# Performance work log

Measured on AMD Instinct MI355X. Metric: run time of the kernel, lower is better.

## Reference

```python
import jax, jax.numpy as jnp
from jax import lax
import numpy as np

NEG = -10000.0

def sequence_mask(length, max_len):
    # [B, max_len] bool
    return jnp.arange(max_len)[None, :] < length[:, None]

def mdn_loss(logp, text_lengths, mel_lengths):
    # logp: [B, T_seq, T_mel]; CTC-style forward recursion over T_mel
    B, T_seq, T_mel = logp.shape
    init = jnp.full((B, T_seq), NEG, logp.dtype).at[:, 0].set(logp[:, 0, 0])
    logp_t = jnp.moveaxis(logp, 2, 0)  # [T_mel, B, T_seq]

    def step(alpha, lp):  # alpha: [B, T_seq]
        shifted = jnp.concatenate(
            [jnp.full((B, 1), NEG, alpha.dtype), alpha[:, :-1]], axis=1)
        new = jnp.logaddexp(alpha + 1e-4, shifted + 1e-4) + lp
        return new, new

    _, cols = lax.scan(step, init, logp_t[1:])
    log_alpha = jnp.concatenate([init[None], cols], axis=0)  # [T_mel, B, T_seq]
    alpha_last = log_alpha[mel_lengths - 1, jnp.arange(B), text_lengths - 1]
    return -alpha_last.mean() / T_seq

def mse_loss_masked(x, target, length):
    # seq_len_norm=False branch: sum of masked squared error / mask.sum() over expanded mask
    B, T, D = x.shape
    mask = sequence_mask(length, T)[:, :, None].astype(x.dtype)  # [B, T, 1]
    diff = x * mask - target * mask
    return jnp.sum(diff * diff) / (jnp.sum(mask) * D)

def sample_wise_min_max(x, mask):
    # x: [B, T, D], mask: [B, T, 1] bool; min/max over dims (1,2)
    maximum = jnp.max(jnp.where(mask, x, 0.0), axis=(1, 2), keepdims=True)
    minimum = jnp.min(jnp.where(mask, x, jnp.inf), axis=(1, 2), keepdims=True)
    return (x - minimum) / (maximum - minimum + 1e-8)

def _gaussian_kernel(size=11, sigma=1.5):
    coords = jnp.arange(size, dtype=jnp.float32) - (size - 1) / 2.0
    g = jnp.exp(-(coords ** 2) / (2.0 * sigma ** 2))
    g = g / g.sum()
    return jnp.outer(g, g)

def _ssim_mean(x, y):
    # x, y: [B, 1, H, W]; 11x11 gaussian SSIM, VALID conv, k1=0.01, k2=0.03, data_range=1
    k = _gaussian_kernel()[None, None].astype(x.dtype)  # [1,1,11,11]
    conv = lambda z: lax.conv_general_dilated(z, k, (1, 1), 'VALID')
    mu_x, mu_y = conv(x), conv(y)
    sxx = conv(x * x) - mu_x * mu_x
    syy = conv(y * y) - mu_y * mu_y
    sxy = conv(x * y) - mu_x * mu_y
    c1, c2 = 0.01 ** 2, 0.03 ** 2
    cs = (2.0 * sxy + c2) / (sxx + syy + c2)
    ssim_map = ((2.0 * mu_x * mu_y + c1) / (mu_x * mu_x + mu_y * mu_y + c1)) * cs
    return ssim_map.mean()

def ssim_loss(y_hat, y, length):
    mask = sequence_mask(length, y.shape[1])[:, :, None]  # [B, T, 1] bool
    y_norm = sample_wise_min_max(y, mask)
    y_hat_norm = sample_wise_min_max(y_hat, mask)
    m = mask.astype(y.dtype)
    loss = 1.0 - _ssim_mean((y_norm * m)[:, None], (y_hat_norm * m)[:, None])
    return jnp.clip(loss, 0.0, 1.0)

SSIM_ALPHA = 1.0
DUR_ALPHA = 1.0
SPEC_ALPHA = 1.0
MDN_ALPHA = 1.0

def setup_inputs() -> dict:
    key = jax.random.key(0)
    ks = jax.random.split(key, 8)
    B, T_seq, T_mel, D = 64, 256, 2048, 80
    logp = jax.random.normal(ks[0], (B, T_seq, T_mel), jnp.float32)
    decoder_output = jax.random.normal(ks[1], (B, T_mel, D), jnp.float32)
    decoder_target = jax.random.uniform(ks[2], (B, T_mel, D), jnp.float32)
    dur_output = jax.random.normal(ks[3], (B, T_seq), jnp.float32)
    dur_target = jax.random.uniform(ks[4], (B, T_seq), jnp.float32)
    decoder_output_lens = jax.random.randint(ks[5], (B,), T_mel // 2, T_mel + 1)
    input_lens = jax.random.randint(ks[6], (B,), T_seq // 2, T_seq + 1)
    return {
        'logp': logp,
        'decoder_output': decoder_output,
        'decoder_target': decoder_target,
        'dur_output': dur_output,
        'dur_target': dur_target,
        'decoder_output_lens': decoder_output_lens,
        'input_lens': input_lens,
        'phase': 4,
    }

def reference(logp, decoder_output, decoder_target, dur_output, dur_target,
              decoder_output_lens, input_lens, phase):
    spec_l = ssim_l = dur_l = mdn_l = 0.0
    if phase == 0:
        mdn_l = mdn_loss(logp, input_lens, decoder_output_lens)
    elif phase == 1:
        spec_l = mse_loss_masked(decoder_output, decoder_target, decoder_output_lens)
        ssim_l = ssim_loss(decoder_output, decoder_target, decoder_output_lens)
    elif phase == 2:
        mdn_l = mdn_loss(logp, input_lens, decoder_output_lens)
        spec_l = mse_loss_masked(decoder_output, decoder_target, decoder_output_lens)
        ssim_l = ssim_loss(decoder_output, decoder_target, decoder_output_lens)
    elif phase == 3:
        dur_l = mse_loss_masked(dur_output[:, :, None], dur_target[:, :, None], input_lens)
    else:
        mdn_l = mdn_loss(logp, input_lens, decoder_output_lens)
        spec_l = mse_loss_masked(decoder_output, decoder_target, decoder_output_lens)
        ssim_l = ssim_loss(decoder_output, decoder_target, decoder_output_lens)
        dur_l = mse_loss_masked(dur_output[:, :, None], dur_target[:, :, None], input_lens)
    loss = SPEC_ALPHA * spec_l + SSIM_ALPHA * ssim_l + DUR_ALPHA * dur_l + MDN_ALPHA * mdn_l
    return loss
```

## Files before the change

kernel.cpp:

```cpp
#include <hip/hip_runtime.h>
#include <math.h>

typedef unsigned short u16;
typedef unsigned int u32;

#define INV_LN2 1.44269504088896f
#define LN2     0.693147180559945f
#define NEG2    (-14426.9504f)


struct Ws {
  double ssim_sum;
  double dur_sum;
  double spec_part[256];
  float  mnT[256], mxT[256], mnO[256], mxO[256];
  float  A[64 * 256];
  float  Bv[64 * 256];
  float  ckF[64 * 256];
  float  ckB[64 * 256];
};

__device__ __forceinline__ float lse2f(float a, float b) {
  float m = fmaxf(a, b);
  float d = fabsf(a - b);
  return m + __builtin_amdgcn_logf(1.0f + __builtin_amdgcn_exp2f(-d));
}
__device__ __forceinline__ float lae2g(float a, float b, float g) {
  float m = fmaxf(a, b);
  float d = fabsf(a - b);
  return (m + g) + __builtin_amdgcn_logf(1.0f + __builtin_amdgcn_exp2f(-d));
}
__device__ __forceinline__ u16 bf16rn(float f) {
  u32 u = __float_as_uint(f);
  u32 r = (u + 0x7fffu + ((u >> 16) & 1u)) >> 16;
  return (u16)r;
}

constexpr float G11[11] = {
  0.00102838f, 0.00759876f, 0.03600077f, 0.10936070f, 0.21300554f,
  0.26601172f,
  0.21300554f, 0.10936070f, 0.03600077f, 0.00759876f, 0.00102838f};

#define TSTR 264
#define TSZ  (32 * TSTR)

__device__ __forceinline__ void stage_tile(const float* __restrict__ gb, int kb,
                                           u16* dst, int tid) {
  const int ltid = tid - 64;
  const int tb = kb << 5;
#pragma unroll
  for (int it = 0; it < 11; ++it) {
    int i = ltid + it * 192;
    if (i < 2048) {
      int s = i >> 3, e = i & 7;
      float4 v = *(const float4*)(gb + (size_t)s * 2048 + tb + 4 * e);
      u16* d = dst + (4 * e) * TSTR + s;
      d[0]        = bf16rn(v.x * INV_LN2);
      d[TSTR]     = bf16rn(v.y * INV_LN2);
      d[2 * TSTR] = bf16rn(v.z * INV_LN2);
      d[3 * TSTR] = bf16rn(v.w * INV_LN2);
    }
  }
}

__global__ __launch_bounds__(256) void kseg1(
    const float* __restrict__ logp,
    const float* __restrict__ deco, const float* __restrict__ dect,
    const float* __restrict__ duro, const float* __restrict__ durt,
    const int* __restrict__ mel_lens, const int* __restrict__ inp_lens,
    Ws* __restrict__ ws) {
  __shared__ u16 TB[2 * TSZ];
  __shared__ float L[5][4];
  const int bid = blockIdx.x, tid = threadIdx.x;
  const int l = tid;

  if (bid < 64) {
    const int b = bid;
    const float* gb = logp + (size_t)b * 256 * 2048;
    float a0 = NEG2, a1 = NEG2, a2 = NEG2, a3 = NEG2;
    if (tid < 64 && l == 0) a0 = gb[0] * INV_LN2;
    auto FWD = [&](uint2 fg) {
      float g0 = __uint_as_float(fg.x << 16);
      float g1 = __uint_as_float(fg.x & 0xffff0000u);
      float g2 = __uint_as_float(fg.y << 16);
      float g3 = __uint_as_float(fg.y & 0xffff0000u);
      int up = __builtin_amdgcn_update_dpp(
          __float_as_int(NEG2), __float_as_int(a3), 0x138, 0xF, 0xF, false);
      float am1 = __int_as_float(up);
      float n0 = lae2g(a0, am1, g0);
      float n1 = lae2g(a1, a0, g1);
      float n2 = lae2g(a2, a1, g2);
      float n3 = lae2g(a3, a2, g3);
      a0 = n0; a1 = n1; a2 = n2; a3 = n3;
    };
    if (tid >= 64) stage_tile(gb, 0, TB, tid);
    __syncthreads();
    if (tid >= 64) stage_tile(gb, 1, TB + TSZ, tid);
    else {
      const u16* fs = TB + 4 * l;
      for (int i = 1; i < 32; ++i) FWD(*(const uint2*)(fs + i * TSTR));
    }
    __syncthreads();
    for (int j = 1; j < 16; ++j) {
      if (tid >= 64) {
        if (j < 15) stage_tile(gb, j + 1, TB + ((j + 1) & 1) * TSZ, tid);
      } else {
        __builtin_amdgcn_s_setprio(1);
        const u16* fs = TB + (j & 1) * TSZ + 4 * l;
        uint2 fb[2][4];
#pragma unroll
        for (int k = 0; k < 4; ++k) fb[0][k] = *(const uint2*)(fs + k * TSTR);
#pragma unroll
        for (int g = 0; g < 8; ++g) {
          const int cur = g & 1, nxt = cur ^ 1;
          if (g < 7) {
#pragma unroll
            for (int k = 0; k < 4; ++k)
              fb[nxt][k] = *(const uint2*)(fs + ((g + 1) * 4 + k) * TSTR);
          }
#pragma unroll
          for (int k = 0; k < 4; ++k) FWD(fb[cur][k]);
        }
        __builtin_amdgcn_s_setprio(0);
      }
      __syncthreads();
    }
    if (tid < 64)
      *(float4*)&ws->ckF[b * 256 + 4 * l] = make_float4(a0, a1, a2, a3);
    return;
  }

  if (bid < 128) {
    const int b = bid - 64;
    const int T = mel_lens[b] - 1;
    const int ss = inp_lens[b] - 1;
    const int kbT = T >> 5;
    const float* gb = logp + (size_t)b * 256 * 2048;
    float b0 = NEG2, b1 = NEG2, b2 = NEG2, b3 = NEG2;
    if (tid < 64) {
      b0 = (4 * l + 0 == ss) ? 0.f : NEG2;
      b1 = (4 * l + 1 == ss) ? 0.f : NEG2;
      b2 = (4 * l + 2 == ss) ? 0.f : NEG2;
      b3 = (4 * l + 3 == ss) ? 0.f : NEG2;
    }
    auto BWD = [&](uint2 bg, bool act) {
      float g0 = __uint_as_float(bg.x << 16);
      float g1 = __uint_as_float(bg.x & 0xffff0000u);
      float g2 = __uint_as_float(bg.y << 16);
      float g3 = __uint_as_float(bg.y & 0xffff0000u);
      float c0 = b0 + g0, c1 = b1 + g1, c2 = b2 + g2, c3 = b3 + g3;
      int dn = __builtin_amdgcn_update_dpp(
          __float_as_int(NEG2), __float_as_int(c0), 0x130, 0xF, 0xF, false);
      float cp = __int_as_float(dn);
      float m0 = lse2f(c0, c1);
      float m1 = lse2f(c1, c2);
      float m2 = lse2f(c2, c3);
      float m3 = lse2f(c3, cp);
      b0 = act ? m0 : b0; b1 = act ? m1 : b1;
      b2 = act ? m2 : b2; b3 = act ? m3 : b3;
    };
    if (tid >= 64) { if (kbT >= 32) stage_tile(gb, kbT, TB, tid); }
    __syncthreads();
    if (tid >= 64) {
      if (kbT - 1 >= 32) stage_tile(gb, kbT - 1, TB + TSZ, tid);
    } else if (kbT >= 32) {
      const u16* bs = TB + 4 * l;
      for (int ii = 31; ii >= 0; --ii) {
        int tt = (kbT << 5) + ii;
        if (tt <= T) BWD(*(const uint2*)(bs + ii * TSTR), true);
      }
    }
    __syncthreads();
    for (int j = 1; j < 16; ++j) {
      if (tid >= 64) {
        int bk = kbT - j - 1;
        if (j < 15 && bk >= 32) stage_tile(gb, bk, TB + ((j + 1) & 1) * TSZ, tid);
      } else {
        __builtin_amdgcn_s_setprio(1);
        const u16* bs = TB + (j & 1) * TSZ + 4 * l;
        const bool act = (kbT - j) >= 32;
        uint2 bb[2][4];
#pragma unroll
        for (int k = 0; k < 4; ++k) bb[0][k] = *(const uint2*)(bs + (31 - k) * TSTR);
#pragma unroll
        for (int g = 0; g < 8; ++g) {
          const int cur = g & 1, nxt = cur ^ 1;
          if (g < 7) {
#pragma unroll
            for (int k = 0; k < 4; ++k)
              bb[nxt][k] = *(const uint2*)(bs + (31 - ((g + 1) * 4 + k)) * TSTR);
          }
#pragma unroll
          for (int k = 0; k < 4; ++k) BWD(bb[cur][k], act);
        }
        __builtin_amdgcn_s_setprio(0);
      }
      __syncthreads();
    }
    if (tid < 64)
      *(float4*)&ws->ckB[b * 256 + 4 * l] = make_float4(b0, b1, b2, b3);
    return;
  }

  if (bid < 384) {
    int idx = bid - 128, b = idx >> 2, part = idx & 3;
    int len = mel_lens[b];
    int rbeg = part * 512;
    int rcnt = len - rbeg; rcnt = rcnt < 0 ? 0 : (rcnt > 512 ? 512 : rcnt);
    float mnT = __builtin_inff(), mxT = -__builtin_inff();
    float mnO = __builtin_inff(), mxO = -__builtin_inff();
    float ssum = 0.f;
    if (rcnt > 0) {
      const float4* po = (const float4*)(deco + ((size_t)(b * 2048 + rbeg)) * 80);
      const float4* pt = (const float4*)(dect + ((size_t)(b * 2048 + rbeg)) * 80);
      int n4 = rcnt * 20;
      for (int i = tid; i < n4; i += 256) {
        float4 vo = po[i], vt = pt[i];
        mnO = fminf(mnO, fminf(fminf(vo.x, vo.y), fminf(vo.z, vo.w)));
        mxO = fmaxf(mxO, fmaxf(fmaxf(vo.x, vo.y), fmaxf(vo.z, vo.w)));
        mnT = fminf(mnT, fminf(fminf(vt.x, vt.y), fminf(vt.z, vt.w)));
        mxT = fmaxf(mxT, fmaxf(fmaxf(vt.x, vt.y), fmaxf(vt.z, vt.w)));
        float dx = vo.x - vt.x, dy = vo.y - vt.y, dz = vo.z - vt.z, dw = vo.w - vt.w;
        ssum += dx * dx + dy * dy + dz * dz + dw * dw;
      }
    }
    for (int o = 32; o; o >>= 1) {
      mnT = fminf(mnT, __shfl_xor(mnT, o));
      mxT = fmaxf(mxT, __shfl_xor(mxT, o));
      mnO = fminf(mnO, __shfl_xor(mnO, o));
      mxO = fmaxf(mxO, __shfl_xor(mxO, o));
      ssum += __shfl_xor(ssum, o);
    }
    int w = tid >> 6;
    if ((tid & 63) == 0) { L[0][w] = mnT; L[1][w] = mxT; L[2][w] = mnO; L[3][w] = mxO; L[4][w] = ssum; }
    __syncthreads();
    if (tid == 0) {
      mnT = fminf(fminf(L[0][0], L[0][1]), fminf(L[0][2], L[0][3]));
      mxT = fmaxf(fmaxf(L[1][0], L[1][1]), fmaxf(L[1][2], L[1][3]));
      mnO = fminf(fminf(L[2][0], L[2][1]), fminf(L[2][2], L[2][3]));
      mxO = fmaxf(fmaxf(L[3][0], L[3][1]), fmaxf(L[3][2], L[3][3]));
      ssum = L[4][0] + L[4][1] + L[4][2] + L[4][3];
      ws->mnT[idx] = mnT; ws->mxT[idx] = mxT; ws->mnO[idx] = mnO; ws->mxO[idx] = mxO;
      ws->spec_part[idx] = (double)ssum;
    }
    return;
  }

  {
    float ssum = 0.f;
    for (int i = tid; i < 64 * 256; i += 256) {
      int b2 = i >> 8, s2 = i & 255;
      if (s2 < inp_lens[b2]) { float d = duro[i] - durt[i]; ssum += d * d; }
    }
    for (int o = 32; o; o >>= 1) ssum += __shfl_xor(ssum, o);
    int w = tid >> 6;
    if ((tid & 63) == 0) L[4][w] = ssum;
    __syncthreads();
    if (tid == 0) {
      ws->dur_sum = (double)(L[4][0] + L[4][1] + L[4][2] + L[4][3]);
      ws->ssim_sum = 0.0;
    }
  }
}

__global__ __launch_bounds__(256) void kseg2(
    const float* __restrict__ logp,
    const float* __restrict__ deco, const float* __restrict__ dect,
    const int* __restrict__ mel_lens, const int* __restrict__ inp_lens,
    Ws* __restrict__ ws) {
  __shared__ float SMF[14704];
  const int bid = blockIdx.x, tid = threadIdx.x;
  const int l = tid;
  u16* TB = (u16*)SMF;

  if (bid < 64) {
    const int b = bid;
    const float* gb = logp + (size_t)b * 256 * 2048;
    float a0 = NEG2, a1 = NEG2, a2 = NEG2, a3 = NEG2;
    if (tid < 64) {
      float4 c = *(const float4*)&ws->ckF[b * 256 + 4 * l];
      a0 = c.x; a1 = c.y; a2 = c.z; a3 = c.w;
    }
    auto FWD = [&](uint2 fg) {
      float g0 = __uint_as_float(fg.x << 16);
      float g1 = __uint_as_float(fg.x & 0xffff0000u);
      float g2 = __uint_as_float(fg.y << 16);
      float g3 = __uint_as_float(fg.y & 0xffff0000u);
      int up = __builtin_amdgcn_update_dpp(
          __float_as_int(NEG2), __float_as_int(a3), 0x138, 0xF, 0xF, false);
      float am1 = __int_as_float(up);
      float n0 = lae2g(a0, am1, g0);
      float n1 = lae2g(a1, a0, g1);
      float n2 = lae2g(a2, a1, g2);
      float n3 = lae2g(a3, a2, g3);
      a0 = n0; a1 = n1; a2 = n2; a3 = n3;
    };
    if (tid >= 64) stage_tile(gb, 16, TB, tid);
    __syncthreads();
    for (int j = 16; j < 32; ++j) {
      if (tid >= 64) {
        if (j < 31) stage_tile(gb, j + 1, TB + ((j + 1) & 1) * TSZ, tid);
      } else {
        __builtin_amdgcn_s_setprio(1);
        const u16* fs = TB + (j & 1) * TSZ + 4 * l;
        uint2 fb[2][4];
#pragma unroll
        for (int k = 0; k < 4; ++k) fb[0][k] = *(const uint2*)(fs + k * TSTR);
#pragma unroll
        for (int g = 0; g < 8; ++g) {
          const int cur = g & 1, nxt = cur ^ 1;
          if (g < 7) {
#pragma unroll
            for (int k = 0; k < 4; ++k)
              fb[nxt][k] = *(const uint2*)(fs + ((g + 1) * 4 + k) * TSTR);
          }
#pragma unroll
          for (int k = 0; k < 4; ++k) FWD(fb[cur][k]);
        }
        __builtin_amdgcn_s_setprio(0);
      }
      __syncthreads();
    }
    if (tid < 64)
      *(float4*)&ws->A[b * 256 + 4 * l] = make_float4(a0, a1, a2, a3);
    return;
  }

  if (bid < 128) {
    const int b = bid - 64;
    const int T = mel_lens[b] - 1;
    const int kbT = T >> 5;
    float b0 = NEG2, b1 = NEG2, b2 = NEG2, b3 = NEG2;
    if (tid < 64) {
      float4 c = *(const float4*)&ws->ckB[b * 256 + 4 * l];
      b0 = c.x; b1 = c.y; b2 = c.z; b3 = c.w;
    }
    if (kbT - 16 < 32) {
      if (tid < 64)
        *(float4*)&ws->Bv[b * 256 + 4 * l] = make_float4(b0, b1, b2, b3);
      return;
    }
    const float* gb = logp + (size_t)b * 256 * 2048;
    auto BWD = [&](uint2 bg, bool act) {
      float g0 = __uint_as_float(bg.x << 16);
      float g1 = __uint_as_float(bg.x & 0xffff0000u);
      float g2 = __uint_as_float(bg.y << 16);
      float g3 = __uint_as_float(bg.y & 0xffff0000u);
      float c0 = b0 + g0, c1 = b1 + g1, c2 = b2 + g2, c3 = b3 + g3;
      int dn = __builtin_amdgcn_update_dpp(
          __float_as_int(NEG2), __float_as_int(c0), 0x130, 0xF, 0xF, false);
      float cp = __int_as_float(dn);
      float m0 = lse2f(c0, c1);
      float m1 = lse2f(c1, c2);
      float m2 = lse2f(c2, c3);
      float m3 = lse2f(c3, cp);
      b0 = act ? m0 : b0; b1 = act ? m1 : b1;
      b2 = act ? m2 : b2; b3 = act ? m3 : b3;
    };
    if (tid >= 64) stage_tile(gb, kbT - 16, TB, tid);
    __syncthreads();
    for (int j = 16; j < 32; ++j) {
      if (tid >= 64) {
        int bk = kbT - j - 1;
        if (j < 31 && bk >= 32) stage_tile(gb, bk, TB + ((j + 1) & 1) * TSZ, tid);
      } else {
        __builtin_amdgcn_s_setprio(1);
        const u16* bs = TB + (j & 1) * TSZ + 4 * l;
        const bool act = (kbT - j) >= 32;
        uint2 bb[2][4];
#pragma unroll
        for (int k = 0; k < 4; ++k) bb[0][k] = *(const uint2*)(bs + (31 - k) * TSTR);
#pragma unroll
        for (int g = 0; g < 8; ++g) {
          const int cur = g & 1, nxt = cur ^ 1;
          if (g < 7) {
#pragma unroll
            for (int k = 0; k < 4; ++k)
              bb[nxt][k] = *(const uint2*)(bs + (31 - ((g + 1) * 4 + k)) * TSTR);
          }
#pragma unroll
          for (int k = 0; k < 4; ++k) BWD(bb[cur][k], act);
        }
        __builtin_amdgcn_s_setprio(0);
      }
      __syncthreads();
    }
    if (tid < 64)
      *(float4*)&ws->Bv[b * 256 + 4 * l] = make_float4(b0, b1, b2, b3);
    return;
  }

  float* cc = SMF;
  float* R = SMF + 14700;
  int cix = bid - 128;
  int b = cix >> 6, tile = cix & 63;
  int r0 = tile * 32;
  int nrows = 2038 - r0; nrows = nrows > 32 ? 32 : nrows;
  int nin = nrows + 10;
  int len = mel_lens[b];

  if (r0 >= len) {
    if (tid == 0) atomicAdd(&ws->ssim_sum, (double)(nrows * 70));
    return;
  }

  float mnT = fminf(fminf(ws->mnT[4 * b], ws->mnT[4 * b + 1]), fminf(ws->mnT[4 * b + 2], ws->mnT[4 * b + 3]));
  float mxT = fmaxf(fmaxf(ws->mxT[4 * b], ws->mxT[4 * b + 1]), fmaxf(ws->mxT[4 * b + 2], ws->mxT[4 * b + 3]));
  float mnO = fminf(fminf(ws->mnO[4 * b], ws->mnO[4 * b + 1]), fminf(ws->mnO[4 * b + 2], ws->mnO[4 * b + 3]));
  float mxO = fmaxf(fmaxf(ws->mxO[4 * b], ws->mxO[4 * b + 1]), fmaxf(ws->mxO[4 * b + 2], ws->mxO[4 * b + 3]));
  if (len < 2048) { mxT = fmaxf(mxT, 0.f); mxO = fmaxf(mxO, 0.f); }
  float sT = 1.0f / (mxT - mnT + 1e-8f);
  float sO = 1.0f / (mxO - mnO + 1e-8f);
  const float* po = deco + (size_t)b * 2048 * 80;
  const float* pt = dect + (size_t)b * 2048 * 80;

  for (int p = tid; p < nin * 70; p += 256) {
    int r = p / 70, j = p - 70 * r;
    int grow = r0 + r;
    float s0 = 0, s1 = 0, s2 = 0, s3 = 0, s4 = 0;
    if (grow < len) {
      const float* ro = po + (size_t)grow * 80 + j;
      const float* rt = pt + (size_t)grow * 80 + j;
#pragma unroll
      for (int k = 0; k < 11; ++k) {
        float tn = (rt[k] - mnT) * sT;
        float on = (ro[k] - mnO) * sO;
        float g = G11[k];
        s0 = fmaf(g, tn, s0);
        s1 = fmaf(g, on, s1);
        s2 = fmaf(g * tn, tn, s2);
        s3 = fmaf(g * on, on, s3);
        s4 = fmaf(g * tn, on, s4);
      }
    }
    cc[p] = s0; cc[2940 + p] = s1; cc[2 * 2940 + p] = s2;
    cc[3 * 2940 + p] = s3; cc[4 * 2940 + p] = s4;
  }
  __syncthreads();

  float acc = 0.f;
  for (int q = tid; q < nrows * 70; q += 256) {
    int i = q / 70, j = q - 70 * i;
    float mx = 0, my = 0, xx = 0, yy = 0, xy = 0;
#pragma unroll
    for (int k = 0; k < 11; ++k) {
      float g = G11[k];
      int o = (i + k) * 70 + j;
      mx = fmaf(g, cc[o], mx);
      my = fmaf(g, cc[2940 + o], my);
      xx = fmaf(g, cc[2 * 2940 + o], xx);
      yy = fmaf(g, cc[3 * 2940 + o], yy);
      xy = fmaf(g, cc[4 * 2940 + o], xy);
    }
    float vx = xx - mx * mx, vy = yy - my * my, vxy = xy - mx * my;
    float cs = (2.f * vxy + 9e-4f) / (vx + vy + 9e-4f);
    float lum = (2.f * mx * my + 1e-4f) / (mx * mx + my * my + 1e-4f);
    acc += lum * cs;
  }
  for (int o = 32; o; o >>= 1) acc += __shfl_xor(acc, o);
  if ((tid & 63) == 0) R[tid >> 6] = acc;
  __syncthreads();
  if (tid == 0) atomicAdd(&ws->ssim_sum, (double)(R[0] + R[1] + R[2] + R[3]));
}

__global__ __launch_bounds__(256) void kfin(
    const int* __restrict__ mel_lens, const int* __restrict__ inp_lens,
    Ws* __restrict__ ws, float* __restrict__ out) {
  __shared__ float MD[64];
  __shared__ double LD[4][4];
  int tid = threadIdx.x;
  {
    int b = tid >> 2, q = tid & 3;
    const float* Ab = ws->A + b * 256;
    const float* Bb = ws->Bv + b * 256;
    float mx = -3.0e38f;
    for (int j = q; j < 256; j += 4) mx = fmaxf(mx, Ab[j] + Bb[j]);
    mx = fmaxf(mx, __shfl_xor(mx, 1));
    mx = fmaxf(mx, __shfl_xor(mx, 2));
    float se = 0.f;
    for (int j = q; j < 256; j += 4)
      se += __builtin_amdgcn_exp2f(Ab[j] + Bb[j] - mx);
    se += __shfl_xor(se, 1);
    se += __shfl_xor(se, 2);
    if (q == 0)
      MD[b] = LN2 * (mx + __builtin_amdgcn_logf(se)) + (float)(mel_lens[b] - 1) * 1e-4f;
  }
  __syncthreads();
  double sp = ws->spec_part[tid];
  double md = 0.0, ml = 0.0, il = 0.0;
  if (tid < 64) {
    md = (double)MD[tid];
    ml = (double)mel_lens[tid];
    il = (double)inp_lens[tid];
  }
  for (int o = 32; o; o >>= 1) {
    sp += __shfl_xor(sp, o);
    md += __shfl_xor(md, o);
    ml += __shfl_xor(ml, o);
    il += __shfl_xor(il, o);
  }
  int w = tid >> 6;
  if ((tid & 63) == 0) { LD[w][0] = sp; LD[w][1] = md; LD[w][2] = ml; LD[w][3] = il; }
  __syncthreads();
  if (tid == 0) {
    sp = LD[0][0] + LD[1][0] + LD[2][0] + LD[3][0];
    md = LD[0][1] + LD[1][1] + LD[2][1] + LD[3][1];
    ml = LD[0][2] + LD[1][2] + LD[2][2] + LD[3][2];
    il = LD[0][3] + LD[1][3] + LD[2][3] + LD[3][3];
    double spec = sp / (ml * 80.0);
    double dur = ws->dur_sum / il;
    double mdn = -(md / 64.0) / 256.0;
    double sm = ws->ssim_sum / (64.0 * 2038.0 * 70.0);
    double sl = 1.0 - sm;
    sl = sl < 0.0 ? 0.0 : (sl > 1.0 ? 1.0 : sl);
    out[0] = (float)(spec + sl + dur + mdn);
  }
}

extern "C" void kernel_launch(void* const* d_in, const int* in_sizes, int n_in,
                              void* d_out, int out_size, void* d_ws, size_t ws_size,
                              hipStream_t stream) {
  const float* logp = (const float*)d_in[0];
  const float* deco = (const float*)d_in[1];
  const float* dect = (const float*)d_in[2];
  const float* duro = (const float*)d_in[3];
  const float* durt = (const float*)d_in[4];
  const int* mel_lens = (const int*)d_in[5];
  const int* inp_lens = (const int*)d_in[6];
  Ws* ws = (Ws*)d_ws;
  hipLaunchKernelGGL(kseg1, dim3(385), dim3(256), 0, stream,
                     logp, deco, dect, duro, durt, mel_lens, inp_lens, ws);
  hipLaunchKernelGGL(kseg2, dim3(128 + 64 * 64), dim3(256), 0, stream,
                     logp, deco, dect, mel_lens, inp_lens, ws);
  hipLaunchKernelGGL(kfin, dim3(1), dim3(256), 0, stream,
                     mel_lens, inp_lens, ws, (float*)d_out);
}
```

Baseline: 181.9 us.

## Widen kseg2 blocks to 512 threads and register-block SSIM horizontal pass

Doubles kseg2's block size to 512 threads. The MDN forward/backward blocks mask off the extra threads so only the original 64 compute and 192 staging threads do work. In the SSIM blocks, the horizontal 11-tap pass now has each thread compute 4 adjacent outputs from 16 vectorized float4 loads, reusing the normalized inputs in registers. The wider block also lets more threads share the vertical pass. The cost is idle threads in the MDN blocks and higher register pressure in the SSIM path, which may reduce occupancy.

```diff
diff --git a/kernel.cpp b/kernel.cpp
--- a/kernel.cpp
+++ b/kernel.cpp
@@ -263,12 +263,12 @@
   }
 }
 
-__global__ __launch_bounds__(256) void kseg2(
+__global__ __launch_bounds__(512) void kseg2(
     const float* __restrict__ logp,
     const float* __restrict__ deco, const float* __restrict__ dect,
     const int* __restrict__ mel_lens, const int* __restrict__ inp_lens,
     Ws* __restrict__ ws) {
-  __shared__ float SMF[14704];
+  __shared__ float SMF[14712];
   const int bid = blockIdx.x, tid = threadIdx.x;
   const int l = tid;
   u16* TB = (u16*)SMF;
@@ -295,12 +295,12 @@
       float n3 = lae2g(a3, a2, g3);
       a0 = n0; a1 = n1; a2 = n2; a3 = n3;
     };
-    if (tid >= 64) stage_tile(gb, 16, TB, tid);
+    if (tid >= 64 && tid < 256) stage_tile(gb, 16, TB, tid);
     __syncthreads();
     for (int j = 16; j < 32; ++j) {
-      if (tid >= 64) {
+      if (tid >= 64 && tid < 256) {
         if (j < 31) stage_tile(gb, j + 1, TB + ((j + 1) & 1) * TSZ, tid);
-      } else {
+      } else if (tid < 64) {
         __builtin_amdgcn_s_setprio(1);
         const u16* fs = TB + (j & 1) * TSZ + 4 * l;
         uint2 fb[2][4];
@@ -357,13 +357,13 @@
       b0 = act ? m0 : b0; b1 = act ? m1 : b1;
       b2 = act ? m2 : b2; b3 = act ? m3 : b3;
     };
-    if (tid >= 64) stage_tile(gb, kbT - 16, TB, tid);
+    if (tid >= 64 && tid < 256) stage_tile(gb, kbT - 16, TB, tid);
     __syncthreads();
     for (int j = 16; j < 32; ++j) {
-      if (tid >= 64) {
+      if (tid >= 64 && tid < 256) {
         int bk = kbT - j - 1;
         if (j < 31 && bk >= 32) stage_tile(gb, bk, TB + ((j + 1) & 1) * TSZ, tid);
-      } else {
+      } else if (tid < 64) {
         __builtin_amdgcn_s_setprio(1);
         const u16* bs = TB + (j & 1) * TSZ + 4 * l;
         const bool act = (kbT - j) >= 32;
@@ -414,33 +414,60 @@
   const float* po = deco + (size_t)b * 2048 * 80;
   const float* pt = dect + (size_t)b * 2048 * 80;
 
-  for (int p = tid; p < nin * 70; p += 256) {
-    int r = p / 70, j = p - 70 * r;
+  for (int task = tid; task < nin * 18; task += 512) {
+    int r = task / 18, q = task - 18 * r;
+    int j0 = q * 4;
     int grow = r0 + r;
-    float s0 = 0, s1 = 0, s2 = 0, s3 = 0, s4 = 0;
+    float sacc[4][5];
+#pragma unroll
+    for (int e = 0; e < 4; ++e)
+#pragma unroll
+      for (int c = 0; c < 5; ++c) sacc[e][c] = 0.f;
     if (grow < len) {
-      const float* ro = po + (size_t)grow * 80 + j;
-      const float* rt = pt + (size_t)grow * 80 + j;
-#pragma unroll
-      for (int k = 0; k < 11; ++k) {
-        float tn = (rt[k] - mnT) * sT;
-        float on = (ro[k] - mnO) * sO;
-        float g = G11[k];
-        s0 = fmaf(g, tn, s0);
-        s1 = fmaf(g, on, s1);
-        s2 = fmaf(g * tn, tn, s2);
-        s3 = fmaf(g * on, on, s3);
-        s4 = fmaf(g * tn, on, s4);
-      }
-    }
-    cc[p] = s0; cc[2940 + p] = s1; cc[2 * 2940 + p] = s2;
-    cc[3 * 2940 + p] = s3; cc[4 * 2940 + p] = s4;
+      const float* rowt = pt + (size_t)grow * 80 + j0;
+      const float* rowo = po + (size_t)grow * 80 + j0;
+      float ft[16], fo[16];
+      *(float4*)&ft[0]  = *(const float4*)(rowt);
+      *(float4*)&ft[4]  = *(const float4*)(rowt + 4);
+      *(float4*)&ft[8]  = *(const float4*)(rowt + 8);
+      *(float4*)&ft[12] = (j0 == 68) ? *(const float4*)(rowt + 8)
+                                     : *(const float4*)(rowt + 12);
+      *(float4*)&fo[0]  = *(const float4*)(rowo);
+      *(float4*)&fo[4]  = *(const float4*)(rowo + 4);
+      *(float4*)&fo[8]  = *(const float4*)(rowo + 8);
+      *(float4*)&fo[12] = (j0 == 68) ? *(const float4*)(rowo + 8)
+                                     : *(const float4*)(rowo + 12);
+#pragma unroll
+      for (int i = 0; i < 16; ++i) {
+        ft[i] = (ft[i] - mnT) * sT;
+        fo[i] = (fo[i] - mnO) * sO;
+      }
+#pragma unroll
+      for (int e = 0; e < 4; ++e) {
+#pragma unroll
+        for (int k = 0; k < 11; ++k) {
+          float tn = ft[e + k], on = fo[e + k], g = G11[k];
+          sacc[e][0] = fmaf(g, tn, sacc[e][0]);
+          sacc[e][1] = fmaf(g, on, sacc[e][1]);
+          sacc[e][2] = fmaf(g * tn, tn, sacc[e][2]);
+          sacc[e][3] = fmaf(g * on, on, sacc[e][3]);
+          sacc[e][4] = fmaf(g * on, tn, sacc[e][4]);
+        }
+      }
+    }
+    int base = r * 70 + j0;
+#pragma unroll
+    for (int c = 0; c < 5; ++c) {
+      *(float2*)&cc[c * 2940 + base] = make_float2(sacc[0][c], sacc[1][c]);
+      if (j0 < 68)
+        *(float2*)&cc[c * 2940 + base + 2] = make_float2(sacc[2][c], sacc[3][c]);
+    }
   }
   __syncthreads();
 
   float acc = 0.f;
-  for (int q = tid; q < nrows * 70; q += 256) {
-    int i = q / 70, j = q - 70 * i;
+  for (int q2 = tid; q2 < nrows * 70; q2 += 512) {
+    int i = q2 / 70, j = q2 - 70 * i;
     float mx = 0, my = 0, xx = 0, yy = 0, xy = 0;
 #pragma unroll
     for (int k = 0; k < 11; ++k) {
@@ -460,7 +487,9 @@
   for (int o = 32; o; o >>= 1) acc += __shfl_xor(acc, o);
   if ((tid & 63) == 0) R[tid >> 6] = acc;
   __syncthreads();
-  if (tid == 0) atomicAdd(&ws->ssim_sum, (double)(R[0] + R[1] + R[2] + R[3]));
+  if (tid == 0)
+    atomicAdd(&ws->ssim_sum,
+              (double)(R[0] + R[1] + R[2] + R[3] + R[4] + R[5] + R[6] + R[7]));
 }
 
 __global__ __launch_bounds__(256) void kfin(
@@ -530,7 +559,7 @@
   Ws* ws = (Ws*)d_ws;
   hipLaunchKernelGGL(kseg1, dim3(385), dim3(256), 0, stream,
                      logp, deco, dect, duro, durt, mel_lens, inp_lens, ws);
-  hipLaunchKernelGGL(kseg2, dim3(128 + 64 * 64), dim3(256), 0, stream,
+  hipLaunchKernelGGL(kseg2, dim3(128 + 64 * 64), dim3(512), 0, stream,
                      logp, deco, dect, mel_lens, inp_lens, ws);
   hipLaunchKernelGGL(kfin, dim3(1), dim3(256), 0, stream,
                      mel_lens, inp_lens, ws, (float*)d_out);
```

Measured after the change: 178.8 us. About the same (-1.7%).
